# Optimization experiments

Hardware: AMD Instinct MI355X
Metric: run time of the kernel (lower is better)

The kernel has to match this reference:

```python
import jax, jax.numpy as jnp
import numpy as np

B, S, E = 4, 2048, 1024
H = 16
HD = E // H  # head_dim = 64


def setup_inputs() -> dict:
    key = jax.random.key(0)
    ks = jax.random.split(key, 12)
    sc = 0.02
    return {
        "q_encodings": jax.random.normal(ks[0], (B, S, E), jnp.float32),
        "k_encodings": jax.random.normal(ks[1], (B, S, E), jnp.float32),
        "v_encodings": jax.random.normal(ks[2], (B, S, E), jnp.float32),
        # per-head q/k/v linear weights [H, HD, HD] and biases [H, HD]
        "Wq": jax.random.normal(ks[3], (H, HD, HD), jnp.float32) * sc,
        "bq": jax.random.normal(ks[4], (H, HD), jnp.float32) * sc,
        "Wk": jax.random.normal(ks[5], (H, HD, HD), jnp.float32) * sc,
        "bk": jax.random.normal(ks[6], (H, HD), jnp.float32) * sc,
        "Wv": jax.random.normal(ks[7], (H, HD, HD), jnp.float32) * sc,
        "bv": jax.random.normal(ks[8], (H, HD), jnp.float32) * sc,
        # output projection [E, E] + bias [E]
        "Wp": jax.random.normal(ks[9], (E, E), jnp.float32) * sc,
        "bp": jax.random.normal(ks[10], (E,), jnp.float32) * sc,
        "mask": 1,
    }


def reference(q_encodings, k_encodings, v_encodings, Wq, bq, Wk, bk, Wv, bv, Wp, bp, mask):
    b, s, e = q_encodings.shape
    h, hd, _ = Wq.shape
    split = lambda x: x.reshape(b, s, h, hd)  # per-head slices of n_embd
    # batched per-head linear projections (original loops over heads)
    Q = jnp.einsum('bshd,hde->bshe', split(q_encodings), Wq) + bq
    K = jnp.einsum('bshd,hde->bshe', split(k_encodings), Wk) + bk
    V = jnp.einsum('bshd,hde->bshe', split(v_encodings), Wv) + bv
    # scaled dot-product scores [B,H,S,S]; scale uses head_dim (Attention.n_embd)
    scores = jnp.einsum('bqhd,bkhd->bhqk', Q, K) / jnp.sqrt(jnp.float32(hd))
    if mask:  # static Python flag, matches torch `if mask:`
        causal = jnp.tril(jnp.ones((s, s), jnp.float32))
        scores = scores + jnp.where(causal == 0, jnp.float32(-jnp.inf), jnp.float32(0.0))
    attn = jax.nn.softmax(scores, axis=-1)
    ctx = jnp.einsum('bhqk,bkhd->bqhd', attn, V).reshape(b, s, e)
    return ctx @ Wp + bp
```

## Files before the change

kernel.cpp:

```cpp
#include <hip/hip_runtime.h>
#include <hip/hip_bf16.h>
#include <math.h>

typedef __bf16 bf16;
typedef __bf16 bf16x8 __attribute__((ext_vector_type(8)));
typedef float f32x4 __attribute__((ext_vector_type(4)));
typedef unsigned int u32x2 __attribute__((ext_vector_type(2)));

constexpr int B = 4, S = 2048, E = 1024, H = 16, HD = 64;

constexpr float QSCALE = 0.125f * 1.44269504088896340736f;

static __device__ __forceinline__ float exp2_fast(float x) {
#if __has_builtin(__builtin_amdgcn_exp2f)
    return __builtin_amdgcn_exp2f(x);
#else
    float r; asm("v_exp_f32 %0, %1" : "=v"(r) : "v"(x)); return r;
#endif
}

static __device__ __forceinline__ unsigned pk_bf16(float a, float b) {
    union { bf16 h[2]; unsigned u; } r;
    r.h[0] = (bf16)a; r.h[1] = (bf16)b;
    return r.u;
}

__global__ __launch_bounds__(256) void prep_wqkv(
    const float* __restrict__ Wq, const float* __restrict__ Wk,
    const float* __restrict__ Wv, bf16* __restrict__ Wt)
{
    const int h = blockIdx.x, p = blockIdx.y;
    const float* W = (p == 0) ? Wq : (p == 1) ? Wk : Wv;
    const float scale = (p == 0) ? QSCALE : 1.0f;
    __shared__ float t[64][65];
    const int tid = threadIdx.x;
    #pragma unroll
    for (int i = 0; i < 16; ++i) {
        int idx = tid + i * 256;
        int d = idx >> 6, e = idx & 63;
        t[d][e] = W[(size_t)h * 4096 + d * 64 + e];
    }
    __syncthreads();
    bf16* dst = Wt + ((size_t)p * H + h) * 4096;
    #pragma unroll
    for (int i = 0; i < 16; ++i) {
        int idx = tid + i * 256;
        int e = idx >> 6, d = idx & 63;
        dst[e * 64 + d] = (bf16)(t[d][e] * scale);
    }
}

__global__ __launch_bounds__(256) void qkv_proj(
    const float* __restrict__ xq, const float* __restrict__ xk, const float* __restrict__ xv,
    const bf16* __restrict__ Wt,
    const float* __restrict__ bq, const float* __restrict__ bk, const float* __restrict__ bv,
    bf16* __restrict__ Qb, bf16* __restrict__ Kb, bf16* __restrict__ Vt)
{
    const int b = blockIdx.z, h = blockIdx.y, s0 = blockIdx.x * 128;
    const int tid = threadIdx.x;
    const int w = tid >> 6, l = tid & 63;
    const int l16 = l & 15, lg = l >> 4;
    const size_t bh = (size_t)b * H + h;

    __shared__ __align__(16) bf16 xs[128][64];
    __shared__ __align__(16) bf16 Wl[64][64];
    __shared__ __align__(16) bf16 ts[10240];

    for (int p = 0; p < 3; ++p) {
        const float* x    = (p == 0) ? xq : (p == 1) ? xk : xv;
        const float* bias = (p == 0) ? bq : (p == 1) ? bk : bv;
        const float  bsc  = (p == 0) ? QSCALE : 1.0f;

        __syncthreads();
        #pragma unroll
        for (int i = 0; i < 4; ++i) {
            int idx = tid + i * 256;
            int r = idx >> 3, g = idx & 7;
            const float* src = &x[((size_t)b * S + s0 + r) * E + h * 64 + g * 8];
            float4 f0 = *(const float4*)src;
            float4 f1 = *(const float4*)(src + 4);
            union { bf16 h8[8]; uint4 u; } pk;
            pk.h8[0] = (bf16)f0.x; pk.h8[1] = (bf16)f0.y;
            pk.h8[2] = (bf16)f0.z; pk.h8[3] = (bf16)f0.w;
            pk.h8[4] = (bf16)f1.x; pk.h8[5] = (bf16)f1.y;
            pk.h8[6] = (bf16)f1.z; pk.h8[7] = (bf16)f1.w;
            *(uint4*)&xs[r][(g ^ (r & 7)) * 8] = pk.u;
        }
        const bf16* wsrc = Wt + ((size_t)p * H + h) * 4096;
        #pragma unroll
        for (int i = 0; i < 2; ++i) {
            int idx = tid + i * 256;
            int e = idx >> 3, g = idx & 7;
            *(uint4*)&Wl[e][(g ^ (e & 7)) * 8] = *(const uint4*)(wsrc + e * 64 + g * 8);
        }
        __syncthreads();

        if (p < 2) {
            float bcol[4];
            #pragma unroll
            for (int ei = 0; ei < 4; ++ei)
                bcol[ei] = bias[h * 64 + ei * 16 + l16] * bsc;
            #pragma unroll
            for (int st = 0; st < 2; ++st) {
                const int srow = w * 32 + st * 16 + l16;
                bf16x8 a0 = *(const bf16x8*)&xs[srow][((lg    ) ^ (srow & 7)) * 8];
                bf16x8 a1 = *(const bf16x8*)&xs[srow][((4 + lg) ^ (srow & 7)) * 8];
                #pragma unroll
                for (int ei = 0; ei < 4; ++ei) {
                    const int erow = ei * 16 + l16;
                    bf16x8 b0 = *(const bf16x8*)&Wl[erow][((lg    ) ^ (erow & 7)) * 8];
                    bf16x8 b1 = *(const bf16x8*)&Wl[erow][((4 + lg) ^ (erow & 7)) * 8];
                    f32x4 acc = {0.f, 0.f, 0.f, 0.f};
                    acc = __builtin_amdgcn_mfma_f32_16x16x32_bf16(a0, b0, acc, 0, 0, 0);
                    acc = __builtin_amdgcn_mfma_f32_16x16x32_bf16(a1, b1, acc, 0, 0, 0);
                    #pragma unroll
                    for (int r = 0; r < 4; ++r)
                        ts[(w * 32 + st * 16 + 4 * lg + r) * 80 + ei * 16 + l16] =
                            (bf16)(acc[r] + bcol[ei]);
                }
            }
            __syncthreads();
            bf16* out = (p == 0) ? Qb : Kb;
            #pragma unroll
            for (int i = 0; i < 4; ++i) {
                int idx = tid + i * 256;
                int r = idx >> 3, g = idx & 7;
                uint4 v = *(const uint4*)&ts[r * 80 + g * 8];
                *(uint4*)(out + (bh * S + s0 + r) * 64 + g * 8) = v;
            }
        } else {
            float brow[4];
            #pragma unroll
            for (int r = 0; r < 4; ++r)
                brow[r] = bias[h * 64 + w * 16 + 4 * lg + r];
            const int erow = w * 16 + l16;
            bf16x8 a0 = *(const bf16x8*)&Wl[erow][((lg    ) ^ (erow & 7)) * 8];
            bf16x8 a1 = *(const bf16x8*)&Wl[erow][((4 + lg) ^ (erow & 7)) * 8];
            #pragma unroll
            for (int st = 0; st < 8; ++st) {
                const int srow = st * 16 + l16;
                bf16x8 b0 = *(const bf16x8*)&xs[srow][((lg    ) ^ (srow & 7)) * 8];
                bf16x8 b1 = *(const bf16x8*)&xs[srow][((4 + lg) ^ (srow & 7)) * 8];
                f32x4 acc = {0.f, 0.f, 0.f, 0.f};
                acc = __builtin_amdgcn_mfma_f32_16x16x32_bf16(a0, b0, acc, 0, 0, 0);
                acc = __builtin_amdgcn_mfma_f32_16x16x32_bf16(a1, b1, acc, 0, 0, 0);
                #pragma unroll
                for (int r = 0; r < 4; ++r)
                    ts[(w * 16 + 4 * lg + r) * 136 + st * 16 + l16] =
                        (bf16)(acc[r] + brow[r]);
            }
            __syncthreads();
            #pragma unroll
            for (int i = 0; i < 4; ++i) {
                int idx = tid + i * 256;
                int r = idx >> 4, g = idx & 15;
                uint4 v = *(const uint4*)&ts[r * 136 + g * 8];
                *(uint4*)(Vt + (bh * 64 + r) * S + s0 + g * 8) = v;
            }
        }
    }
}

__global__ __launch_bounds__(256) void prep_wp(const float* __restrict__ Wp,
                                               bf16* __restrict__ Wpt)
{
    __shared__ float t[64][65];
    const int tid = threadIdx.x;
    const int k0 = blockIdx.y * 64, n0 = blockIdx.x * 64;
    #pragma unroll
    for (int i = 0; i < 16; ++i) {
        int idx = tid + i * 256;
        int r = idx >> 6, c = idx & 63;
        t[r][c] = Wp[(size_t)(k0 + r) * E + n0 + c];
    }
    __syncthreads();
    #pragma unroll
    for (int i = 0; i < 16; ++i) {
        int idx = tid + i * 256;
        int r = idx >> 6, c = idx & 63;
        Wpt[(size_t)(n0 + r) * E + k0 + c] = (bf16)t[c][r];
    }
}

__global__ __launch_bounds__(512) void attn(
    const bf16* __restrict__ Qb, const bf16* __restrict__ Kb,
    const bf16* __restrict__ Vt, bf16* __restrict__ ctx)
{
    const int pair = blockIdx.x;
    const int bh   = blockIdx.y;
    const int b = bh >> 4, h = bh & 15;
    const int tid = threadIdx.x;
    const int w = tid >> 6;
    const int l = tid & 63;
    const int l16 = l & 15, lg = l >> 4;

    __shared__ __align__(16) bf16 Kl[2][64][64];
    __shared__ __align__(16) bf16 Vl[2][64][64];
    __shared__ __align__(16) bf16 Pl[8][16][72];

    const bf16* Qp = Qb + (size_t)bh * S * 64;
    const bf16* Kp = Kb + (size_t)bh * S * 64;
    const bf16* Vp = Vt + (size_t)bh * 64 * S;

    const int str = tid >> 3;
    const int stc = tid & 7;
    const int sws = (stc ^ (str & 7)) * 8;

    #pragma unroll 1
    for (int half = 0; half < 2; ++half) {
        const int qt   = half ? (15 - pair) : pair;
        const int qw0  = qt * 128 + w * 16;
        const int qabs = qw0 + l16;
        const int nt   = 2 * qt + 2;

        bf16x8 qf0 = *(const bf16x8*)(Qp + (size_t)qabs * 64 + lg * 8);
        bf16x8 qf1 = *(const bf16x8*)(Qp + (size_t)qabs * 64 + 32 + lg * 8);

        f32x4 o[4] = {};
        float m_run = -1e30f, l_run = 0.f;

        {
            uint4 kreg = *(const uint4*)(Kp + (size_t)str * 64 + stc * 8);
            uint4 vreg = *(const uint4*)(Vp + (size_t)str * S + stc * 8);
            *(uint4*)&Kl[0][str][sws] = kreg;
            *(uint4*)&Vl[0][str][sws] = vreg;
        }
        int cur = 0;
        for (int t = 0; t < nt; ++t) {
            __syncthreads();
            const bool pfv = (t + 1 < nt);
            uint4 kreg, vreg;
            if (pfv) {
                const int kv1 = (t + 1) * 64;
                kreg = *(const uint4*)(Kp + (size_t)(kv1 + str) * 64 + stc * 8);
                vreg = *(const uint4*)(Vp + (size_t)str * S + kv1 + stc * 8);
            }
            const int kv0 = t * 64;
            if (kv0 < qw0 + 16) {
                float p[16];
                #pragma unroll
                for (int s = 0; s < 4; ++s) {
                    f32x4 sc = {0.f, 0.f, 0.f, 0.f};
                    const int row = 16 * s + l16;
                    bf16x8 ka = *(const bf16x8*)&Kl[cur][row][(lg       ^ (l16 & 7)) * 8];
                    bf16x8 kb = *(const bf16x8*)&Kl[cur][row][((4 + lg) ^ (l16 & 7)) * 8];
                    sc = __builtin_amdgcn_mfma_f32_16x16x32_bf16(ka, qf0, sc, 0, 0, 0);
                    sc = __builtin_amdgcn_mfma_f32_16x16x32_bf16(kb, qf1, sc, 0, 0, 0);
                    p[4 * s + 0] = sc[0]; p[4 * s + 1] = sc[1];
                    p[4 * s + 2] = sc[2]; p[4 * s + 3] = sc[3];
                }

                if (kv0 + 63 > qw0) {
                    #pragma unroll
                    for (int i = 0; i < 16; ++i) {
                        const int kvloc = 16 * (i >> 2) + 4 * lg + (i & 3);
                        if (kv0 + kvloc > qabs) p[i] = -1e30f;
                    }
                }

                float mx = p[0];
                #pragma unroll
                for (int i = 1; i < 16; ++i) mx = fmaxf(mx, p[i]);
                mx = fmaxf(mx, __shfl_xor(mx, 16));
                mx = fmaxf(mx, __shfl_xor(mx, 32));
                const float m_new = fmaxf(m_run, mx);
                const float corr = exp2_fast(m_run - m_new);
                float sum = 0.f;
                #pragma unroll
                for (int i = 0; i < 16; ++i) { p[i] = exp2_fast(p[i] - m_new); sum += p[i]; }
                sum += __shfl_xor(sum, 16);
                sum += __shfl_xor(sum, 32);
                l_run = l_run * corr + sum;
                m_run = m_new;
                #pragma unroll
                for (int ds = 0; ds < 4; ++ds) {
                    o[ds][0] *= corr; o[ds][1] *= corr;
                    o[ds][2] *= corr; o[ds][3] *= corr;
                }

                #pragma unroll
                for (int s = 0; s < 4; ++s) {
                    u32x2 pw;
                    pw[0] = pk_bf16(p[4 * s + 0], p[4 * s + 1]);
                    pw[1] = pk_bf16(p[4 * s + 2], p[4 * s + 3]);
                    *(u32x2*)&Pl[w][l16][16 * s + 4 * lg] = pw;
                }
                asm volatile("s_waitcnt lgkmcnt(0)" ::: "memory");
                bf16x8 pf0 = *(const bf16x8*)&Pl[w][l16][8 * lg];
                bf16x8 pf1 = *(const bf16x8*)&Pl[w][l16][32 + 8 * lg];

                #pragma unroll
                for (int ds = 0; ds < 4; ++ds) {
                    const int row = 16 * ds + l16;
                    bf16x8 v0 = *(const bf16x8*)&Vl[cur][row][(lg       ^ (l16 & 7)) * 8];
                    bf16x8 v1 = *(const bf16x8*)&Vl[cur][row][((4 + lg) ^ (l16 & 7)) * 8];
                    o[ds] = __builtin_amdgcn_mfma_f32_16x16x32_bf16(v0, pf0, o[ds], 0, 0, 0);
                    o[ds] = __builtin_amdgcn_mfma_f32_16x16x32_bf16(v1, pf1, o[ds], 0, 0, 0);
                }
            }
            if (pfv) {
                *(uint4*)&Kl[cur ^ 1][str][sws] = kreg;
                *(uint4*)&Vl[cur ^ 1][str][sws] = vreg;
            }
            cur ^= 1;
        }

        const float il = 1.0f / l_run;
        bf16* crow = ctx + ((size_t)b * S + qabs) * E + h * 64;
        #pragma unroll
        for (int ds = 0; ds < 4; ++ds) {
            u32x2 pw;
            pw[0] = pk_bf16(o[ds][0] * il, o[ds][1] * il);
            pw[1] = pk_bf16(o[ds][2] * il, o[ds][3] * il);
            *(u32x2*)(crow + 16 * ds + 4 * lg) = pw;
        }
    }
}

__global__ __launch_bounds__(256) void out_gemm(
    const bf16* __restrict__ A, const bf16* __restrict__ Bt,
    const float* __restrict__ bp, float* __restrict__ C)
{
    const int n0 = blockIdx.x * 128, m0 = blockIdx.y * 128;
    const int tid = threadIdx.x;
    const int w = tid >> 6, l = tid & 63;
    const int l16 = l & 15, lg = l >> 4;
    const int wm = w >> 1, wn = w & 1;

    __shared__ __align__(16) bf16 Al[128][64];
    __shared__ __align__(16) bf16 Bl[128][64];

    f32x4 acc[4][4] = {};

    for (int k0 = 0; k0 < E; k0 += 64) {
        __syncthreads();
        #pragma unroll
        for (int i = 0; i < 4; ++i) {
            int row = (tid >> 3) + i * 32;
            int c = tid & 7;
            int cs = c ^ (row & 7);
            *(uint4*)&Al[row][cs * 8] =
                *(const uint4*)(A + (size_t)(m0 + row) * E + k0 + c * 8);
            *(uint4*)&Bl[row][cs * 8] =
                *(const uint4*)(Bt + (size_t)(n0 + row) * E + k0 + c * 8);
        }
        __syncthreads();

        #pragma unroll
        for (int ks = 0; ks < 2; ++ks) {
            bf16x8 af[4], bfr[4];
            #pragma unroll
            for (int mi = 0; mi < 4; ++mi) {
                int r = wm * 64 + mi * 16 + l16;
                af[mi] = *(const bf16x8*)&Al[r][((ks * 4 + lg) ^ (r & 7)) * 8];
            }
            #pragma unroll
            for (int ni = 0; ni < 4; ++ni) {
                int r = wn * 64 + ni * 16 + l16;
                bfr[ni] = *(const bf16x8*)&Bl[r][((ks * 4 + lg) ^ (r & 7)) * 8];
            }
            #pragma unroll
            for (int mi = 0; mi < 4; ++mi)
                #pragma unroll
                for (int ni = 0; ni < 4; ++ni)
                    acc[mi][ni] = __builtin_amdgcn_mfma_f32_16x16x32_bf16(
                        af[mi], bfr[ni], acc[mi][ni], 0, 0, 0);
        }
    }

    #pragma unroll
    for (int ni = 0; ni < 4; ++ni) {
        const int col = n0 + wn * 64 + ni * 16 + l16;
        const float bias = bp[col];
        #pragma unroll
        for (int mi = 0; mi < 4; ++mi) {
            #pragma unroll
            for (int e = 0; e < 4; ++e) {
                int row = m0 + wm * 64 + mi * 16 + 4 * lg + e;
                C[(size_t)row * E + col] = acc[mi][ni][e] + bias;
            }
        }
    }
}

extern "C" void kernel_launch(void* const* d_in, const int* in_sizes, int n_in,
                              void* d_out, int out_size, void* d_ws, size_t ws_size,
                              hipStream_t stream)
{
    const float* xq = (const float*)d_in[0];
    const float* xk = (const float*)d_in[1];
    const float* xv = (const float*)d_in[2];
    const float* Wq = (const float*)d_in[3];
    const float* bq = (const float*)d_in[4];
    const float* Wk = (const float*)d_in[5];
    const float* bk = (const float*)d_in[6];
    const float* Wv = (const float*)d_in[7];
    const float* bv = (const float*)d_in[8];
    const float* Wp = (const float*)d_in[9];
    const float* bp = (const float*)d_in[10];
    float* out = (float*)d_out;

    char* ws = (char*)d_ws;
    const size_t sz_bhse = (size_t)B * H * S * HD;
    bf16* Qb  = (bf16*)ws;  ws += sz_bhse * 2;
    bf16* Kb  = (bf16*)ws;  ws += sz_bhse * 2;
    bf16* Vtw = (bf16*)ws;  ws += sz_bhse * 2;
    bf16* ctx = (bf16*)ws;  ws += (size_t)B * S * E * 2;
    bf16* Wpt = (bf16*)ws;  ws += (size_t)E * E * 2;
    bf16* Wt3 = (bf16*)ws;  ws += (size_t)3 * H * HD * HD * 2;

    prep_wqkv<<<dim3(H, 3), 256, 0, stream>>>(Wq, Wk, Wv, Wt3);
    qkv_proj<<<dim3(S / 128, H, B), 256, 0, stream>>>(xq, xk, xv, Wt3,
                                                      bq, bk, bv, Qb, Kb, Vtw);
    prep_wp<<<dim3(E / 64, E / 64), 256, 0, stream>>>(Wp, Wpt);
    attn<<<dim3(8, B * H), 512, 0, stream>>>(Qb, Kb, Vtw, ctx);
    out_gemm<<<dim3(E / 128, (B * S) / 128), 256, 0, stream>>>(ctx, Wpt, bp, out);
}
```

Measured before the change: 132.2 us.

## Add lazy softmax rescaling, MFMA priority hints, and double-buffer output GEMM

In the attention kernel, the running max and rescale of the output accumulators are now updated only when some lane's new max exceeds the old one by more than a threshold of 11.5 (in log2 units). This skips most per-tile correction multiplies, at the cost of relying on bf16/fp32 headroom for the unnormalised exponentials. The kernel also precomputes swizzled LDS offsets and wraps the MFMA sections in s_setprio hints. The output projection GEMM gains a register-staged double-buffered LDS pipeline, so global loads of the next K tile overlap the current tile's MFMAs and one barrier per iteration is removed.

```diff
diff --git a/kernel.cpp b/kernel.cpp
--- a/kernel.cpp
+++ b/kernel.cpp
@@ -10,6 +10,7 @@
 constexpr int B = 4, S = 2048, E = 1024, H = 16, HD = 64;
 
 constexpr float QSCALE = 0.125f * 1.44269504088896340736f;
+constexpr float DTHR = 11.5f;
 
 static __device__ __forceinline__ float exp2_fast(float x) {
 #if __has_builtin(__builtin_amdgcn_exp2f)
@@ -206,6 +207,16 @@
     const int stc = tid & 7;
     const int sws = (stc ^ (str & 7)) * 8;
 
+    int foff0[4], foff1[4];
+    #pragma unroll
+    for (int s = 0; s < 4; ++s) {
+        foff0[s] = (16 * s + l16) * 64 + ((lg    ) ^ (l16 & 7)) * 8;
+        foff1[s] = (16 * s + l16) * 64 + ((4 + lg) ^ (l16 & 7)) * 8;
+    }
+    bf16* Plw = &Pl[w][0][0];
+    const int pwr = l16 * 72 + 4 * lg;
+    const int prd = l16 * 72 + 8 * lg;
+
     #pragma unroll 1
     for (int half = 0; half < 2; ++half) {
         const int qt   = half ? (15 - pair) : pair;
@@ -237,18 +248,22 @@
             }
             const int kv0 = t * 64;
             if (kv0 < qw0 + 16) {
+                const bf16* Kbase = &Kl[cur][0][0];
+                const bf16* Vbase = &Vl[cur][0][0];
+
                 float p[16];
+                __builtin_amdgcn_s_setprio(1);
                 #pragma unroll
                 for (int s = 0; s < 4; ++s) {
                     f32x4 sc = {0.f, 0.f, 0.f, 0.f};
-                    const int row = 16 * s + l16;
-                    bf16x8 ka = *(const bf16x8*)&Kl[cur][row][(lg       ^ (l16 & 7)) * 8];
-                    bf16x8 kb = *(const bf16x8*)&Kl[cur][row][((4 + lg) ^ (l16 & 7)) * 8];
+                    bf16x8 ka = *(const bf16x8*)(Kbase + foff0[s]);
+                    bf16x8 kb = *(const bf16x8*)(Kbase + foff1[s]);
                     sc = __builtin_amdgcn_mfma_f32_16x16x32_bf16(ka, qf0, sc, 0, 0, 0);
                     sc = __builtin_amdgcn_mfma_f32_16x16x32_bf16(kb, qf1, sc, 0, 0, 0);
                     p[4 * s + 0] = sc[0]; p[4 * s + 1] = sc[1];
                     p[4 * s + 2] = sc[2]; p[4 * s + 3] = sc[3];
                 }
+                __builtin_amdgcn_s_setprio(0);
 
                 if (kv0 + 63 > qw0) {
                     #pragma unroll
@@ -263,40 +278,44 @@
                 for (int i = 1; i < 16; ++i) mx = fmaxf(mx, p[i]);
                 mx = fmaxf(mx, __shfl_xor(mx, 16));
                 mx = fmaxf(mx, __shfl_xor(mx, 32));
-                const float m_new = fmaxf(m_run, mx);
-                const float corr = exp2_fast(m_run - m_new);
+                if (!__all(mx <= m_run + DTHR)) {
+                    const float m_new = fmaxf(m_run, mx);
+                    const float corr = exp2_fast(m_run - m_new);
+                    l_run *= corr;
+                    #pragma unroll
+                    for (int ds = 0; ds < 4; ++ds) {
+                        o[ds][0] *= corr; o[ds][1] *= corr;
+                        o[ds][2] *= corr; o[ds][3] *= corr;
+                    }
+                    m_run = m_new;
+                }
                 float sum = 0.f;
                 #pragma unroll
-                for (int i = 0; i < 16; ++i) { p[i] = exp2_fast(p[i] - m_new); sum += p[i]; }
+                for (int i = 0; i < 16; ++i) { p[i] = exp2_fast(p[i] - m_run); sum += p[i]; }
                 sum += __shfl_xor(sum, 16);
                 sum += __shfl_xor(sum, 32);
-                l_run = l_run * corr + sum;
-                m_run = m_new;
-                #pragma unroll
-                for (int ds = 0; ds < 4; ++ds) {
-                    o[ds][0] *= corr; o[ds][1] *= corr;
-                    o[ds][2] *= corr; o[ds][3] *= corr;
-                }
+                l_run += sum;
 
                 #pragma unroll
                 for (int s = 0; s < 4; ++s) {
                     u32x2 pw;
                     pw[0] = pk_bf16(p[4 * s + 0], p[4 * s + 1]);
                     pw[1] = pk_bf16(p[4 * s + 2], p[4 * s + 3]);
-                    *(u32x2*)&Pl[w][l16][16 * s + 4 * lg] = pw;
+                    *(u32x2*)(Plw + pwr + 16 * s) = pw;
                 }
                 asm volatile("s_waitcnt lgkmcnt(0)" ::: "memory");
-                bf16x8 pf0 = *(const bf16x8*)&Pl[w][l16][8 * lg];
-                bf16x8 pf1 = *(const bf16x8*)&Pl[w][l16][32 + 8 * lg];
-
+                bf16x8 pf0 = *(const bf16x8*)(Plw + prd);
+                bf16x8 pf1 = *(const bf16x8*)(Plw + prd + 32);
+
+                __builtin_amdgcn_s_setprio(1);
                 #pragma unroll
                 for (int ds = 0; ds < 4; ++ds) {
-                    const int row = 16 * ds + l16;
-                    bf16x8 v0 = *(const bf16x8*)&Vl[cur][row][(lg       ^ (l16 & 7)) * 8];
-                    bf16x8 v1 = *(const bf16x8*)&Vl[cur][row][((4 + lg) ^ (l16 & 7)) * 8];
+                    bf16x8 v0 = *(const bf16x8*)(Vbase + foff0[ds]);
+                    bf16x8 v1 = *(const bf16x8*)(Vbase + foff1[ds]);
                     o[ds] = __builtin_amdgcn_mfma_f32_16x16x32_bf16(v0, pf0, o[ds], 0, 0, 0);
                     o[ds] = __builtin_amdgcn_mfma_f32_16x16x32_bf16(v1, pf1, o[ds], 0, 0, 0);
                 }
+                __builtin_amdgcn_s_setprio(0);
             }
             if (pfv) {
                 *(uint4*)&Kl[cur ^ 1][str][sws] = kreg;
@@ -327,37 +346,50 @@
     const int l16 = l & 15, lg = l >> 4;
     const int wm = w >> 1, wn = w & 1;
 
-    __shared__ __align__(16) bf16 Al[128][64];
-    __shared__ __align__(16) bf16 Bl[128][64];
+    __shared__ __align__(16) bf16 Al[2][128][64];
+    __shared__ __align__(16) bf16 Bl[2][128][64];
 
     f32x4 acc[4][4] = {};
 
+    const int row_ = tid >> 3;
+    const int c_   = tid & 7;
+    const int cs   = (c_ ^ (row_ & 7)) * 8;
+
+    uint4 apre[4], bpre[4];
+    #pragma unroll
+    for (int i = 0; i < 4; ++i) {
+        apre[i] = *(const uint4*)(A  + (size_t)(m0 + row_ + i * 32) * E + c_ * 8);
+        bpre[i] = *(const uint4*)(Bt + (size_t)(n0 + row_ + i * 32) * E + c_ * 8);
+    }
+    #pragma unroll
+    for (int i = 0; i < 4; ++i) {
+        *(uint4*)&Al[0][row_ + i * 32][cs] = apre[i];
+        *(uint4*)&Bl[0][row_ + i * 32][cs] = bpre[i];
+    }
+
+    int cur = 0;
     for (int k0 = 0; k0 < E; k0 += 64) {
         __syncthreads();
-        #pragma unroll
-        for (int i = 0; i < 4; ++i) {
-            int row = (tid >> 3) + i * 32;
-            int c = tid & 7;
-            int cs = c ^ (row & 7);
-            *(uint4*)&Al[row][cs * 8] =
-                *(const uint4*)(A + (size_t)(m0 + row) * E + k0 + c * 8);
-            *(uint4*)&Bl[row][cs * 8] =
-                *(const uint4*)(Bt + (size_t)(n0 + row) * E + k0 + c * 8);
-        }
-        __syncthreads();
-
+        const bool pfv = (k0 + 64 < E);
+        if (pfv) {
+            #pragma unroll
+            for (int i = 0; i < 4; ++i) {
+                apre[i] = *(const uint4*)(A  + (size_t)(m0 + row_ + i * 32) * E + k0 + 64 + c_ * 8);
+                bpre[i] = *(const uint4*)(Bt + (size_t)(n0 + row_ + i * 32) * E + k0 + 64 + c_ * 8);
+            }
+        }
         #pragma unroll
         for (int ks = 0; ks < 2; ++ks) {
             bf16x8 af[4], bfr[4];
             #pragma unroll
             for (int mi = 0; mi < 4; ++mi) {
                 int r = wm * 64 + mi * 16 + l16;
-                af[mi] = *(const bf16x8*)&Al[r][((ks * 4 + lg) ^ (r & 7)) * 8];
+                af[mi] = *(const bf16x8*)&Al[cur][r][((ks * 4 + lg) ^ (r & 7)) * 8];
             }
             #pragma unroll
             for (int ni = 0; ni < 4; ++ni) {
                 int r = wn * 64 + ni * 16 + l16;
-                bfr[ni] = *(const bf16x8*)&Bl[r][((ks * 4 + lg) ^ (r & 7)) * 8];
+                bfr[ni] = *(const bf16x8*)&Bl[cur][r][((ks * 4 + lg) ^ (r & 7)) * 8];
             }
             #pragma unroll
             for (int mi = 0; mi < 4; ++mi)
@@ -366,6 +398,14 @@
                     acc[mi][ni] = __builtin_amdgcn_mfma_f32_16x16x32_bf16(
                         af[mi], bfr[ni], acc[mi][ni], 0, 0, 0);
         }
+        if (pfv) {
+            #pragma unroll
+            for (int i = 0; i < 4; ++i) {
+                *(uint4*)&Al[cur ^ 1][row_ + i * 32][cs] = apre[i];
+                *(uint4*)&Bl[cur ^ 1][row_ + i * 32][cs] = bpre[i];
+            }
+        }
+        cur ^= 1;
     }
 
     #pragma unroll
```

After: 171.4 us. +29.7%, slower.
